# Performance work log

Measured on AMD Instinct MI355X. Metric: run time of the kernel, lower is better.

## Reference

```python
import jax, jax.numpy as jnp
import numpy as np

B, CIN, NH, W, L, K = 16, 64, 64, 32, 4, 5
EPS = 1e-5
FORGET_BIAS = 1.0


def conv(x, w, b=None):
    # x: [B,C,H,W], w: [O,I,k,k] -> SAME padding, stride 1 (NCHW)
    y = jax.lax.conv_general_dilated(x, w, (1, 1), 'SAME',
                                     dimension_numbers=('NCHW', 'OIHW', 'NCHW'))
    if b is not None:
        y = y + b[None, :, None, None]
    return y


def ln(x, g, b):
    # torch LayerNorm([C,W,W]): normalize each sample over (C,H,W)
    m = jnp.mean(x, axis=(1, 2, 3), keepdims=True)
    v = jnp.mean((x - m) ** 2, axis=(1, 2, 3), keepdims=True)
    return (x - m) * jax.lax.rsqrt(v + EPS) * g[None] + b[None]


def attn_channel(q, kv):
    # q: [B,C,W,H], kv: [B,L,C,W,H]
    b, c, w, h = q.shape
    qf = q.reshape(b, c, w * h)                 # [B,C,HW]
    kf = kv.reshape(b, -1, w * h)               # [B,L*C,HW]
    a = jax.nn.softmax(jnp.einsum('bcp,blp->bcl', qf, kf), axis=2)  # [B,C,L*C]
    out = jnp.einsum('bcl,blp->bcp', a, kf)     # [B,C,HW]
    return out.reshape(b, c, w, h)


def attn_spatial(q, kv):
    # q: [B,C,W,H], kv: [B,L,C,W,H]
    b, c, w, h = q.shape
    qf = q.reshape(b, c, w * h).transpose(0, 2, 1)          # [B,HW,C]
    kf = kv.transpose(0, 1, 3, 4, 2).reshape(b, -1, c)      # [B,L*HW,C]
    a = jax.nn.softmax(jnp.einsum('bpc,bqc->bpq', qf, kf), axis=2)  # [B,HW,L*HW]
    out = jnp.einsum('bpq,bqc->bpc', a, kf)                 # [B,HW,C]
    return out.reshape(b, w, h, c).transpose(0, 3, 1, 2)


def setup_inputs() -> dict:
    key = jax.random.key(0)
    ks = iter(jax.random.split(key, 64))
    rn = lambda shape, s=1.0: jax.random.normal(next(ks), shape, jnp.float32) * s
    ones = lambda shape: jnp.ones(shape, jnp.float32)
    zeros = lambda shape: jnp.zeros(shape, jnp.float32)
    s = 0.02
    d = {}
    d['x_t'] = rn((B, CIN, W, W))
    d['h_t'] = rn((B, NH, W, W))
    d['c_t'] = rn((B, NH, W, W))
    d['c_historys'] = rn((B, L, NH, W, W))
    d['m_t'] = rn((B, NH, W, W))
    d['w_x'] = rn((7 * NH, CIN, K, K), s); d['ln_x_g'] = ones((7 * NH, W, W)); d['ln_x_b'] = zeros((7 * NH, W, W))
    d['w_h'] = rn((4 * NH, NH, K, K), s);  d['ln_h_g'] = ones((4 * NH, W, W)); d['ln_h_b'] = zeros((4 * NH, W, W))
    d['w_m'] = rn((3 * NH, NH, K, K), s);  d['ln_m_g'] = ones((3 * NH, W, W)); d['ln_m_b'] = zeros((3 * NH, W, W))
    d['w_o'] = rn((NH, 2 * NH, K, K), s);  d['ln_o_g'] = ones((NH, W, W));     d['ln_o_b'] = zeros((NH, W, W))
    d['w_last'] = rn((NH, 2 * NH, 1, 1), s)
    d['s_norm_g'] = ones((NH, W, W)); d['s_norm_b'] = zeros((NH, W, W))
    d['c_norm_g'] = ones((NH, W, W)); d['c_norm_b'] = zeros((NH, W, W))
    d['ca_w1'] = rn((NH, NH, K, K), s); d['ca_b1'] = zeros((NH,))
    d['ca_ln_g'] = ones((NH, W, W));    d['ca_ln_b'] = zeros((NH, W, W))
    d['ca_w2'] = rn((NH, NH, 1, 1), s); d['ca_b2'] = zeros((NH,))
    d['sa_w1'] = rn((NH, NH, K, K), s)
    d['sa_ln_g'] = ones((NH, W, W));    d['sa_ln_b'] = zeros((NH, W, W))
    d['sa_w2'] = rn((NH, NH, 1, 1), s)
    d['attn_w'] = rn((NH, NH, 1, 1), s)
    return d


def reference(x_t, h_t, c_t, c_historys, m_t,
              w_x, ln_x_g, ln_x_b, w_h, ln_h_g, ln_h_b, w_m, ln_m_g, ln_m_b,
              w_o, ln_o_g, ln_o_b, w_last,
              s_norm_g, s_norm_b, c_norm_g, c_norm_b,
              ca_w1, ca_b1, ca_ln_g, ca_ln_b, ca_w2, ca_b2,
              sa_w1, sa_ln_g, sa_ln_b, sa_w2, attn_w):
    x_concat = ln(conv(x_t, w_x), ln_x_g, ln_x_b)
    h_concat = ln(conv(h_t, w_h), ln_h_g, ln_h_b)
    m_concat = ln(conv(m_t, w_m), ln_m_g, ln_m_b)
    (i_x, f_x, g_x, i_xp, f_xp, g_xp, o_x) = jnp.split(x_concat, 7, axis=1)
    (i_h, f_h, g_h, o_h) = jnp.split(h_concat, 4, axis=1)
    (i_m, f_m, g_m) = jnp.split(m_concat, 3, axis=1)

    i_t = jax.nn.sigmoid(i_x + i_h)
    f_t = jax.nn.sigmoid(f_x + f_h + FORGET_BIAS)
    g_t = jnp.tanh(g_x + g_h)

    # attn_sum_fussion(c_t, query=f_t, keys=c_historys, values=c_historys)
    sp = ln(c_t + attn_spatial(f_t, c_historys), s_norm_g, s_norm_b)
    ch = ln(c_t + attn_channel(f_t, c_historys), c_norm_g, c_norm_b)
    s_a = conv(jax.nn.relu(ln(conv(sp, sa_w1), sa_ln_g, sa_ln_b)), sa_w2)
    c_a = conv(jax.nn.relu(ln(conv(ch, ca_w1, ca_b1), ca_ln_g, ca_ln_b)), ca_w2, ca_b2)
    attn = conv(s_a + c_a, attn_w)
    c_new = attn + i_t * g_t

    i_tp = jax.nn.sigmoid(i_xp + i_m)
    f_tp = jax.nn.sigmoid(f_xp + f_m + FORGET_BIAS)
    g_tp = jnp.tanh(g_xp + g_m)
    m_new = f_tp * m_t + i_tp * g_tp

    mem = jnp.concatenate((c_new, m_new), axis=1)
    o_t = jax.nn.sigmoid(o_x + o_h + ln(conv(mem, w_o), ln_o_g, ln_o_b))
    h_new = o_t * jnp.tanh(conv(mem, w_last))
    return h_new, c_new, m_new
```

## Files before the change

kernel.cpp:

```cpp
#include <hip/hip_runtime.h>
#include <hip/hip_bf16.h>

#define N1 (1u << 20)

typedef __attribute__((ext_vector_type(8))) short s8v;
typedef __attribute__((ext_vector_type(4))) float f4v;

static __device__ __forceinline__ float sigm(float x){ return 1.f/(1.f + __expf(-x)); }
static __device__ __forceinline__ float tanh_(float x){ return 1.f - 2.f/(__expf(2.f*x) + 1.f); }

static __device__ __forceinline__ ushort f2b(float f){
  union { float f; uint u; } x; x.f = f;
  uint r = x.u + 0x7FFFu + ((x.u >> 16) & 1u);
  return (ushort)(r >> 16);
}

static __device__ __forceinline__ void red_atomic2(float s, float q, float* d, int b, int t){
  #pragma unroll
  for (int m = 32; m; m >>= 1){ s += __shfl_xor(s, m); q += __shfl_xor(q, m); }
  if ((t & 63) == 0){ atomicAdd(&d[b*2], s); atomicAdd(&d[b*2+1], q); }
}

__global__ __launch_bounds__(256) void k_wprep3(
    const float* __restrict__ sA, ushort* __restrict__ dA, int CoA, int CiA, int nA,
    const float* __restrict__ sB, ushort* __restrict__ dB, int CoB, int CiB, int nB,
    const float* __restrict__ sC, ushort* __restrict__ dC, int CoC, int CiC, int nC,
    float* __restrict__ zs)
{
  if (zs && blockIdx.x == 0) zs[threadIdx.x] = 0.f;
  int idx = blockIdx.x*256 + threadIdx.x;
  const float* s; ushort* d; int Co, Ci;
  if (idx < nA){ s=sA; d=dA; Co=CoA; Ci=CiA; }
  else if ((idx -= nA) < nB){ s=sB; d=dB; Co=CoB; Ci=CiB; }
  else if ((idx -= nB) < nC){ s=sC; d=dC; Co=CoC; Ci=CiC; }
  else return;
  int ci = idx % Ci; int r = idx / Ci; int co = r % Co; int tap = r / Co;
  d[idx] = f2b(s[((size_t)(co*Ci + ci))*25 + tap]);
}

struct PT { const float* s; ushort* d; const float* st; const float* g; const float* bb; };

__global__ __launch_bounds__(256) void k_prepT3(PT ja, PT jb, PT jc, int n0, int n1, float invN)
{
  const int lp = blockIdx.y;
  PT j; int pl;
  if (lp < n0){ j = ja; pl = lp; }
  else if (lp < n0 + n1){ j = jb; pl = lp - n0; }
  else { j = jc; pl = lp - n0 - n1; }
  const float* sp = j.s + ((size_t)pl << 16);
  float mean = 0.f, rstd = 0.f;
  if (j.st){
    float s0 = j.st[pl*2], s1 = j.st[pl*2+1];
    mean = s0*invN; rstd = rsqrtf(s1*invN - mean*mean + 1e-5f);
  }
  const int p0 = blockIdx.x << 6;
  __shared__ __align__(16) float T[64][68];
  const int t = threadIdx.x, c = t >> 2, g4 = t & 3;
  #pragma unroll
  for (int i = 0; i < 4; ++i){
    const int px = (g4 << 4) + (i << 2);
    float4 f = *(const float4*)(sp + ((size_t)c << 10) + p0 + px);
    if (j.st){
      const size_t li = ((size_t)c << 10) + p0 + px;
      float4 gv = *(const float4*)(j.g + li);
      float4 bv = *(const float4*)(j.bb + li);
      f.x = (f.x - mean)*rstd*gv.x + bv.x;
      f.y = (f.y - mean)*rstd*gv.y + bv.y;
      f.z = (f.z - mean)*rstd*gv.z + bv.z;
      f.w = (f.w - mean)*rstd*gv.w + bv.w;
    }
    *(float4*)&T[c][px] = f;
  }
  __syncthreads();
  const int p = t >> 2, c0 = (t & 3) << 4;
  uint w4[8];
  #pragma unroll
  for (int k = 0; k < 8; ++k){
    ushort lo = f2b(T[c0 + 2*k][p]);
    ushort hi = f2b(T[c0 + 2*k + 1][p]);
    w4[k] = (uint)lo | ((uint)hi << 16);
  }
  ushort* dst = j.d + ((((size_t)pl << 10) + p0 + p) << 6) + c0;
  *(uint4*)(dst)     = *(uint4*)&w4[0];
  *(uint4*)(dst + 8) = *(uint4*)&w4[4];
}

__global__ __launch_bounds__(256) void k_prepTm(const float* __restrict__ src, ushort* __restrict__ dT)
{
  const int lp = blockIdx.y;
  const int p0 = blockIdx.x << 6;
  const float* sp = src + ((size_t)lp << 16);
  __shared__ __align__(16) float T[64][68];
  const int t = threadIdx.x, c = t >> 2, g4 = t & 3;
  #pragma unroll
  for (int i = 0; i < 4; ++i){
    const int px = (g4 << 4) + (i << 2);
    *(float4*)&T[c][px] = *(const float4*)(sp + ((size_t)c << 10) + p0 + px);
  }
  __syncthreads();
  const int p = t >> 2, c0 = (t & 3) << 4;
  uint w4[8];
  #pragma unroll
  for (int k = 0; k < 8; ++k)
    w4[k] = (uint)f2b(T[c0 + 2*k][p]) | ((uint)f2b(T[c0 + 2*k + 1][p]) << 16);
  ushort* dst = dT + ((((size_t)(lp >> 1) << 10) + p0 + p) << 7) + ((lp & 1) << 6) + c0;
  *(uint4*)(dst)     = *(uint4*)&w4[0];
  *(uint4*)(dst + 8) = *(uint4*)&w4[4];
}

struct Seg {
  const ushort* inT; const ushort* w; const float* bias;
  float* out; float* ostat;
  int Cin, Cout;
};
struct Segs3 { Seg s[3]; int b1, b2; };

template<int MT, int RPB>
__global__ __launch_bounds__(256, MT==4 ? 2 : 3) void k_convX(Segs3 Sg)
{
  constexpr int CO   = MT*16;
  constexpr int NW   = 5*CO*4;
  constexpr int ITW  = (NW + 255) / 256;
  constexpr int DXSH = (MT == 4 ? 8 : 7);
  constexpr int PXB  = 32/RPB;
  constexpr int ROWS = RPB + 4;
  constexpr int RPW  = RPB/4;
  constexpr int NTIL = RPB/2;
  constexpr int SUN2 = ROWS*36;

  const int b = blockIdx.y;
  const int cog = blockIdx.x / PXB, pxblk = blockIdx.x % PXB;
  const int si = (cog >= Sg.b1) + (cog >= Sg.b2);
  const Seg sg = Sg.s[si];
  const int base = si == 0 ? 0 : (si == 1 ? Sg.b1 : Sg.b2);
  const int co0 = (cog - base) * CO;
  const int r0 = pxblk * RPB;
  const int t = threadIdx.x, w = t >> 6, l = t & 63;
  const int lane16 = l & 15, quad = l >> 4;

  __shared__ __align__(16) ushort S_[4][ROWS][36][8];
  __shared__ __align__(16) ushort W_[2][5*CO*32];

  f4v acc[MT][NTIL];
  #pragma unroll
  for (int mi = 0; mi < MT; ++mi)
    #pragma unroll
    for (int n = 0; n < NTIL; ++n) acc[mi][n] = (f4v){0.f,0.f,0.f,0.f};

  size_t woff0[ITW];
  #pragma unroll
  for (int it = 0; it < ITW; ++it){
    const int u = t + it*256;
    const int l16u = u & 15, qu = (u >> 4) & 3;
    const int miu = (u >> 6) & (MT - 1), dxu = u >> DXSH;
    woff0[it] = ((size_t)(dxu*sg.Cout + co0 + miu*16 + l16u))*sg.Cin + (qu << 3);
  }
  const size_t wdy = (size_t)5 * sg.Cout * sg.Cin;

  const int ncc = sg.Cin >> 5;
  for (int cc = 0; cc < ncc; ++cc){
    __syncthreads();
    for (int idx = t; idx < SUN2; idx += 256){
      const int row = idx / 36, col = idx - row*36;
      const int ir = r0 - 2 + row, ic = col - 2;
      uint4 pk[4] = {make_uint4(0,0,0,0),make_uint4(0,0,0,0),make_uint4(0,0,0,0),make_uint4(0,0,0,0)};
      if ((unsigned)ir < 32u && (unsigned)ic < 32u){
        const ushort* bp = sg.inT + ((size_t)((b << 10) + (ir << 5) + ic)) * sg.Cin + (cc << 5);
        #pragma unroll
        for (int q = 0; q < 4; ++q) pk[q] = *(const uint4*)(bp + (q << 3));
      }
      #pragma unroll
      for (int q = 0; q < 4; ++q) *(uint4*)&S_[q][row][col][0] = pk[q];
    }
    {
      uint4 wreg[ITW];
      #pragma unroll
      for (int it = 0; it < ITW; ++it)
        if (ITW*256 == NW || t + it*256 < NW)
          wreg[it] = *(const uint4*)(sg.w + woff0[it] + (cc << 5));
      #pragma unroll
      for (int it = 0; it < ITW; ++it)
        if (ITW*256 == NW || t + it*256 < NW)
          *(uint4*)&W_[0][(size_t)(t + it*256) * 8] = wreg[it];
    }
    __syncthreads();
    #pragma unroll
    for (int dy = 0; dy < 5; ++dy){
      uint4 nreg[ITW];
      if (dy < 4){
        #pragma unroll
        for (int it = 0; it < ITW; ++it)
          if (ITW*256 == NW || t + it*256 < NW)
            nreg[it] = *(const uint4*)(sg.w + woff0[it] + (size_t)(dy+1)*wdy + (cc << 5));
      }
      #pragma unroll
      for (int dx = 0; dx < 5; ++dx){
        s8v a[MT];
        #pragma unroll
        for (int mi = 0; mi < MT; ++mi){
          const int au = ((((dx*MT + mi) << 2) + quad) << 4) + lane16;
          a[mi] = *(const s8v*)&W_[dy & 1][au << 3];
        }
        #pragma unroll
        for (int n = 0; n < NTIL; ++n){
          const int srow = w*RPW + (n >> 1) + dy;
          const int col = ((n & 1) << 4) + lane16 + dx;
          s8v bb = *(const s8v*)&S_[quad][srow][col][0];
          #pragma unroll
          for (int mi = 0; mi < MT; ++mi)
            acc[mi][n] = __builtin_amdgcn_mfma_f32_16x16x32_bf16(a[mi], bb, acc[mi][n], 0, 0, 0);
        }
      }
      if (dy < 4){
        #pragma unroll
        for (int it = 0; it < ITW; ++it)
          if (ITW*256 == NW || t + it*256 < NW)
            *(uint4*)&W_[(dy+1) & 1][(size_t)(t + it*256) * 8] = nreg[it];
      }
      __syncthreads();
    }
  }
  float lsum = 0.f, lsq = 0.f;
  #pragma unroll
  for (int mi = 0; mi < MT; ++mi){
    const int co = co0 + mi*16 + (quad << 2);
    #pragma unroll
    for (int n = 0; n < NTIL; ++n){
      const int row = r0 + w*RPW + (n >> 1);
      const int col = ((n & 1) << 4) + lane16;
      #pragma unroll
      for (int i = 0; i < 4; ++i){
        float v = acc[mi][n][i] + (sg.bias ? sg.bias[co+i] : 0.f);
        sg.out[(((size_t)(b*sg.Cout + co + i)) << 10) + (row << 5) + col] = v;
        lsum += v; lsq += v*v;
      }
    }
  }
  if (sg.ostat) red_atomic2(lsum, lsq, sg.ostat, b, t);
}

__global__ __launch_bounds__(256) void k_prep2(
    const float* __restrict__ sA, ushort* __restrict__ cA, ushort* __restrict__ tA, int nA,
    const float* __restrict__ sB, ushort* __restrict__ cB, ushort* __restrict__ tB)
{
  const int plane = blockIdx.y;
  const float* src; ushort* outC; ushort* outT; int pl;
  if (plane < nA){ src = sA; outC = cA; outT = tA; pl = plane; }
  else { src = sB; outC = cB; outT = tB; pl = plane - nA; }
  const int p0 = blockIdx.x << 6;
  const float* sp = src + ((size_t)pl << 16);
  __shared__ __align__(16) float T[64][68];
  const int t = threadIdx.x, c = t >> 2, g = t & 3;
  #pragma unroll
  for (int i = 0; i < 4; ++i){
    float4 f = *(const float4*)(sp + ((size_t)c << 10) + p0 + (g << 4) + (i << 2));
    *(float4*)&T[c][(g << 4) + (i << 2)] = f;
    uint2 pk2;
    pk2.x = (uint)f2b(f.x) | ((uint)f2b(f.y) << 16);
    pk2.y = (uint)f2b(f.z) | ((uint)f2b(f.w) << 16);
    *(uint2*)(outC + ((((size_t)pl << 6) + c) << 10) + p0 + (g << 4) + (i << 2)) = pk2;
  }
  __syncthreads();
  const int p = t >> 2, c0 = (t & 3) << 4;
  uint w4[8];
  #pragma unroll
  for (int k = 0; k < 8; ++k){
    ushort lo = f2b(T[c0 + 2*k][p]);
    ushort hi = f2b(T[c0 + 2*k + 1][p]);
    w4[k] = (uint)lo | ((uint)hi << 16);
  }
  ushort* dst = outT + ((((size_t)pl << 10) + p0 + p) << 6) + c0;
  *(uint4*)(dst)     = *(uint4*)&w4[0];
  *(uint4*)(dst + 8) = *(uint4*)&w4[4];
}

__global__ __launch_bounds__(256) void k_gates(
    const float* __restrict__ bufx, const float* __restrict__ bufh, const float* __restrict__ bufm,
    const float* __restrict__ lnxg, const float* __restrict__ lnxb,
    const float* __restrict__ lnhg, const float* __restrict__ lnhb,
    const float* __restrict__ lnmg, const float* __restrict__ lnmb,
    const float* __restrict__ m_t, const float* __restrict__ stats,
    float* __restrict__ ft, float* __restrict__ ig, float* __restrict__ osum,
    float* __restrict__ memo, float* __restrict__ out_m)
{
  const int idx = blockIdx.x*256 + threadIdx.x;
  const int b = idx >> 16, rem = idx & 65535;
  const int c = rem >> 10, p = rem & 1023;

  float mx = stats[b*2]      * (1.f/458752.f);
  float vx = stats[b*2+1]    * (1.f/458752.f) - mx*mx;  float rx = rsqrtf(vx + 1e-5f);
  float mh = stats[32+b*2]   * (1.f/262144.f);
  float vh = stats[32+b*2+1] * (1.f/262144.f) - mh*mh;  float rh = rsqrtf(vh + 1e-5f);
  float mm = stats[64+b*2]   * (1.f/196608.f);
  float vm = stats[64+b*2+1] * (1.f/196608.f) - mm*mm;  float rm = rsqrtf(vm + 1e-5f);

  auto LX = [&](int k){
    size_t ch = (size_t)k*64 + c; size_t gi = ((size_t)b*448 + ch)*1024 + p; size_t li = ch*1024 + p;
    return (bufx[gi] - mx)*rx*lnxg[li] + lnxb[li]; };
  auto LH = [&](int k){
    size_t ch = (size_t)k*64 + c; size_t gi = ((size_t)b*256 + ch)*1024 + p; size_t li = ch*1024 + p;
    return (bufh[gi] - mh)*rh*lnhg[li] + lnhb[li]; };
  auto LM = [&](int k){
    size_t ch = (size_t)k*64 + c; size_t gi = ((size_t)b*192 + ch)*1024 + p; size_t li = ch*1024 + p;
    return (bufm[gi] - mm)*rm*lnmg[li] + lnmb[li]; };

  float i_t = sigm(LX(0) + LH(0));
  float f_t = sigm(LX(1) + LH(1) + 1.f);
  float g_t = tanh_(LX(2) + LH(2));
  float i_p = sigm(LX(3) + LM(0));
  float f_p = sigm(LX(4) + LM(1) + 1.f);
  float g_p = tanh_(LX(5) + LM(2));
  float ox = LX(6), oh = LH(3);

  ft[idx]   = f_t;
  ig[idx]   = i_t * g_t;
  osum[idx] = ox + oh;
  float mn = f_p * m_t[idx] + i_p * g_p;
  out_m[idx] = mn;
  memo[((size_t)(b*128 + 64 + c) << 10) + p] = mn;
}

__global__ __launch_bounds__(256) void k_spat_mfma(
    const ushort* __restrict__ qT, const ushort* __restrict__ kvC, const ushort* __restrict__ kvT,
    float* __restrict__ num, float* __restrict__ den)
{
  const int p0 = blockIdx.x << 6, b = blockIdx.y, half = blockIdx.z;
  const int t = threadIdx.x, w = t >> 6, l = t & 63;
  const int lane16 = l & 15, quad = l >> 4;
  __shared__ __align__(16) ushort Kt[64][72];
  __shared__ __align__(16) ushort Kc[64][72];
  __shared__ __align__(16) ushort Eb[64][72];
  __shared__ __align__(16) float  XO[64][65];

  s8v qa0, qa1;
  {
    const ushort* qr = qT + ((((size_t)b << 10) + p0 + (w << 4) + lane16) << 6) + (quad << 3);
    qa0 = *(const s8v*)(qr);
    qa1 = *(const s8v*)(qr + 32);
  }
  f4v o0 = {0.f,0.f,0.f,0.f}, o1 = o0, o2 = o0, o3 = o0, dacc = o0;
  const short oneb = (short)0x3F80;
  const s8v ones = { oneb, oneb, oneb, oneb, oneb, oneb, oneb, oneb };

  const int r = t >> 2, g4 = (t & 3) << 4;
  for (int ck = 0; ck < 16; ++ck){
    const int chunk = (half << 4) + ck;
    const int lidx = chunk >> 4, pk = (chunk & 15) << 6;
    __syncthreads();
    {
      const ushort* sc = kvC + ((((size_t)(b*4 + lidx) << 6) + r) << 10) + pk + g4;
      *(uint4*)&Kc[r][g4]     = *(const uint4*)(sc);
      *(uint4*)&Kc[r][g4 + 8] = *(const uint4*)(sc + 8);
      const ushort* st = kvT + ((((size_t)(b*4 + lidx) << 10) + pk + r) << 6) + g4;
      *(uint4*)&Kt[r][g4]     = *(const uint4*)(st);
      *(uint4*)&Kt[r][g4 + 8] = *(const uint4*)(st + 8);
    }
    __syncthreads();
    #pragma unroll
    for (int nt = 0; nt < 4; ++nt){
      const ushort* bt = &Kt[(nt << 4) + lane16][quad << 3];
      s8v b0 = *(const s8v*)(bt);
      s8v b1 = *(const s8v*)(bt + 32);
      f4v s = {0.f,0.f,0.f,0.f};
      s = __builtin_amdgcn_mfma_f32_16x16x32_bf16(qa0, b0, s, 0, 0, 0);
      s = __builtin_amdgcn_mfma_f32_16x16x32_bf16(qa1, b1, s, 0, 0, 0);
      #pragma unroll
      for (int i = 0; i < 4; ++i){
        float e = __expf(s[i] - 12.f);
        Eb[(w << 4) + (quad << 2) + i][(nt << 4) + lane16] = f2b(e);
      }
    }
    __syncthreads();
    #pragma unroll
    for (int ks = 0; ks < 2; ++ks){
      s8v ea = *(const s8v*)&Eb[(w << 4) + lane16][(ks << 5) + (quad << 3)];
      dacc = __builtin_amdgcn_mfma_f32_16x16x32_bf16(ea, ones, dacc, 0, 0, 0);
      s8v bc0 = *(const s8v*)&Kc[ 0 + lane16][(ks << 5) + (quad << 3)];
      s8v bc1 = *(const s8v*)&Kc[16 + lane16][(ks << 5) + (quad << 3)];
      s8v bc2 = *(const s8v*)&Kc[32 + lane16][(ks << 5) + (quad << 3)];
      s8v bc3 = *(const s8v*)&Kc[48 + lane16][(ks << 5) + (quad << 3)];
      o0 = __builtin_amdgcn_mfma_f32_16x16x32_bf16(ea, bc0, o0, 0, 0, 0);
      o1 = __builtin_amdgcn_mfma_f32_16x16x32_bf16(ea, bc1, o1, 0, 0, 0);
      o2 = __builtin_amdgcn_mfma_f32_16x16x32_bf16(ea, bc2, o2, 0, 0, 0);
      o3 = __builtin_amdgcn_mfma_f32_16x16x32_bf16(ea, bc3, o3, 0, 0, 0);
    }
  }
  {
    const int pxl = (w << 4) + (quad << 2);
    if (lane16 == 0){
      float* dp = den + (((size_t)(half*16 + b)) << 10) + p0 + pxl;
      dp[0] = dacc[0]; dp[1] = dacc[1]; dp[2] = dacc[2]; dp[3] = dacc[3];
    }
    XO[ 0 + lane16][pxl+0] = o0[0]; XO[ 0 + lane16][pxl+1] = o0[1];
    XO[ 0 + lane16][pxl+2] = o0[2]; XO[ 0 + lane16][pxl+3] = o0[3];
    XO[16 + lane16][pxl+0] = o1[0]; XO[16 + lane16][pxl+1] = o1[1];
    XO[16 + lane16][pxl+2] = o1[2]; XO[16 + lane16][pxl+3] = o1[3];
    XO[32 + lane16][pxl+0] = o2[0]; XO[32 + lane16][pxl+1] = o2[1];
    XO[32 + lane16][pxl+2] = o2[2]; XO[32 + lane16][pxl+3] = o2[3];
    XO[48 + lane16][pxl+0] = o3[0]; XO[48 + lane16][pxl+1] = o3[1];
    XO[48 + lane16][pxl+2] = o3[2]; XO[48 + lane16][pxl+3] = o3[3];
  }
  __syncthreads();
  {
    const int ch = t >> 2;
    float* nout = num + (size_t)half * N1;
    #pragma unroll
    for (int i = 0; i < 4; ++i){
      size_t gi = ((size_t)b << 16) + ((size_t)ch << 10) + p0 + g4 + (i << 2);
      float4 ov;
      ov.x = XO[ch][g4 + (i << 2) + 0];
      ov.y = XO[ch][g4 + (i << 2) + 1];
      ov.z = XO[ch][g4 + (i << 2) + 2];
      ov.w = XO[ch][g4 + (i << 2) + 3];
      *(float4*)(nout + gi) = ov;
    }
  }
}

__global__ __launch_bounds__(256) void k_spcomb(
    const float* num, const float* __restrict__ den,
    const float* __restrict__ c_t, float* sp_raw, float* __restrict__ stats)
{
  const int p0 = blockIdx.x << 6, b = blockIdx.y, t = threadIdx.x;
  const int ch = t >> 2, g4 = (t & 3) << 4;
  float lsum = 0.f, lsq = 0.f;
  #pragma unroll
  for (int i = 0; i < 4; ++i){
    const int px = p0 + g4 + (i << 2);
    size_t gi = ((size_t)b << 16) + ((size_t)ch << 10) + px;
    float4 ns = {0.f,0.f,0.f,0.f};
    float d0 = 0.f, d1 = 0.f, d2 = 0.f, d3 = 0.f;
    #pragma unroll
    for (int k = 0; k < 4; ++k){
      float4 nk = *(const float4*)(num + (size_t)k*N1 + gi);
      ns.x += nk.x; ns.y += nk.y; ns.z += nk.z; ns.w += nk.w;
      const float* dp = den + (((size_t)(k*16 + b)) << 10) + px;
      d0 += dp[0]; d1 += dp[1]; d2 += dp[2]; d3 += dp[3];
    }
    float4 cv = *(const float4*)(c_t + gi);
    float4 ov;
    ov.x = cv.x + ns.x / d0;
    ov.y = cv.y + ns.y / d1;
    ov.z = cv.z + ns.z / d2;
    ov.w = cv.w + ns.w / d3;
    *(float4*)(sp_raw + gi) = ov;
    lsum += ov.x + ov.y + ov.z + ov.w;
    lsq  += ov.x*ov.x + ov.y*ov.y + ov.z*ov.z + ov.w*ov.w;
  }
  red_atomic2(lsum, lsq, stats, b, t);
}

__global__ __launch_bounds__(256) void k_chlog_m(
    const ushort* __restrict__ ftC, const ushort* __restrict__ kvC, float* __restrict__ lg)
{
  const int bx = blockIdx.x, b = blockIdx.y;
  const int np = bx >> 1, mp = bx & 1;
  const int t = threadIdx.x, w = t >> 6, l = t & 63;
  const int lane16 = l & 15, quad = l >> 4;
  __shared__ __align__(16) ushort As[8][32][8];
  __shared__ __align__(16) ushort Bs[8][64][8];
  f4v acc[2];
  acc[0] = (f4v){0.f,0.f,0.f,0.f}; acc[1] = (f4v){0.f,0.f,0.f,0.f};

  for (int kc = 0; kc < 16; ++kc){
    __syncthreads();
    {
      const int c = t >> 3, q = t & 7;
      *(uint4*)&As[q][c][0] = *(const uint4*)(ftC + (((size_t)(b*64 + mp*32 + c)) << 10) + (kc<<6) + (q<<3));
    }
    #pragma unroll
    for (int it = 0; it < 2; ++it){
      const int idx = t + it*256;
      const int r2 = idx >> 3, q = idx & 7;
      *(uint4*)&Bs[q][r2][0] = *(const uint4*)(kvC + ((((size_t)(b*4 + np) << 6) + r2) << 10) + (kc<<6) + (q<<3));
    }
    __syncthreads();
    #pragma unroll
    for (int ks = 0; ks < 2; ++ks){
      s8v a0 = *(const s8v*)&As[(ks<<2)+quad][lane16][0];
      s8v a1 = *(const s8v*)&As[(ks<<2)+quad][16 + lane16][0];
      s8v bb = *(const s8v*)&Bs[(ks<<2)+quad][(w<<4) + lane16][0];
      acc[0] = __builtin_amdgcn_mfma_f32_16x16x32_bf16(a0, bb, acc[0], 0, 0, 0);
      acc[1] = __builtin_amdgcn_mfma_f32_16x16x32_bf16(a1, bb, acc[1], 0, 0, 0);
    }
  }
  #pragma unroll
  for (int mi = 0; mi < 2; ++mi)
    #pragma unroll
    for (int i = 0; i < 4; ++i){
      const int c = mp*32 + mi*16 + (quad<<2) + i;
      const int n = (np<<6) + (w<<4) + lane16;
      lg[(((size_t)(b*64 + c)) << 8) + n] = acc[mi][i];
    }
}

__global__ __launch_bounds__(256) void k_chsm(const float* __restrict__ a, ushort* __restrict__ ab)
{
  const int row  = blockIdx.x*4 + (threadIdx.x >> 6);
  const int lane = threadIdx.x & 63;
  const float* rp = a + ((size_t)row << 8);
  float v0 = rp[lane], v1 = rp[lane+64], v2 = rp[lane+128], v3 = rp[lane+192];
  float mx = fmaxf(fmaxf(v0, v1), fmaxf(v2, v3));
  #pragma unroll
  for (int m = 32; m; m >>= 1) mx = fmaxf(mx, __shfl_xor(mx, m));
  v0 = __expf(v0 - mx); v1 = __expf(v1 - mx); v2 = __expf(v2 - mx); v3 = __expf(v3 - mx);
  float s = v0 + v1 + v2 + v3;
  #pragma unroll
  for (int m = 32; m; m >>= 1) s += __shfl_xor(s, m);
  float inv = 1.f / s;
  ushort* op = ab + ((size_t)row << 8);
  op[lane] = f2b(v0*inv); op[lane+64] = f2b(v1*inv);
  op[lane+128] = f2b(v2*inv); op[lane+192] = f2b(v3*inv);
}

__global__ __launch_bounds__(256) void k_chout_m(
    const ushort* __restrict__ chlb, const ushort* __restrict__ kvT,
    const float* __restrict__ c_t, float* __restrict__ ch_raw, float* __restrict__ stats)
{
  const int p0 = blockIdx.x << 6, b = blockIdx.y;
  const int t = threadIdx.x, w = t >> 6, l = t & 63;
  const int lane16 = l & 15, quad = l >> 4;
  __shared__ __align__(16) ushort As[32][64][8];
  __shared__ __align__(16) ushort Bs[32][32][8];
  #pragma unroll
  for (int it = 0; it < 8; ++it){
    const int idx = t + it*256;
    const int c = idx >> 5, q = idx & 31;
    *(uint4*)&As[q][c][0] = *(const uint4*)(chlb + (((size_t)(b*64 + c)) << 8) + (q<<3));
  }
  __syncthreads();
  s8v a[8];
  #pragma unroll
  for (int ks = 0; ks < 8; ++ks)
    a[ks] = *(const s8v*)&As[(ks<<2)+quad][(w<<4) + lane16][0];
  float lsum = 0.f, lsq = 0.f;
  for (int pc = 0; pc < 2; ++pc){
    __syncthreads();
    #pragma unroll
    for (int it = 0; it < 4; ++it){
      const int idx = t + it*256;
      const int px = idx >> 5, q = idx & 31;
      const int plane = (b<<2) + (q>>3);
      *(uint4*)&Bs[q][px][0] = *(const uint4*)(kvT + ((((size_t)plane << 10) + p0 + (pc<<5) + px) << 6) + ((q&7)<<3));
    }
    __syncthreads();
    #pragma unroll
    for (int nt = 0; nt < 2; ++nt){
      f4v o = {0.f,0.f,0.f,0.f};
      #pragma unroll
      for (int ks = 0; ks < 8; ++ks){
        s8v bb = *(const s8v*)&Bs[(ks<<2)+quad][(nt<<4) + lane16][0];
        o = __builtin_amdgcn_mfma_f32_16x16x32_bf16(a[ks], bb, o, 0, 0, 0);
      }
      #pragma unroll
      for (int i = 0; i < 4; ++i){
        const int c = (w<<4) + (quad<<2) + i;
        const int px = p0 + (pc<<5) + (nt<<4) + lane16;
        size_t gi = ((size_t)b << 16) + ((size_t)c << 10) + px;
        float v = c_t[gi] + o[i];
        ch_raw[gi] = v;
        lsum += v; lsq += v*v;
      }
    }
  }
  red_atomic2(lsum, lsq, stats, b, t);
}

__global__ __launch_bounds__(256) void k_attnfinal(
    const float* __restrict__ samid, const float* __restrict__ camid,
    const float* __restrict__ stats_sa, const float* __restrict__ stats_ca,
    const float* __restrict__ salng, const float* __restrict__ salnb,
    const float* __restrict__ calng, const float* __restrict__ calnb,
    const float* __restrict__ wsa2, const float* __restrict__ wca2,
    const float* __restrict__ cab2, const float* __restrict__ wat,
    const float* __restrict__ ig, float* __restrict__ out_c, float* __restrict__ memo)
{
  const int p0 = blockIdx.x << 6, b = blockIdx.y, t = threadIdx.x;
  const int tc = t & 15, tp = t >> 4;
  __shared__ __align__(16) float R[64][68];
  __shared__ __align__(16) float Wl[64][68];
  __shared__ __align__(16) float Ms[64][68];
  const float invN = 1.f/65536.f;
  float acc[4][4] = {};
  #pragma unroll
  for (int pass = 0; pass < 2; ++pass){
    const float* mid = pass ? camid : samid;
    const float* st  = pass ? stats_ca : stats_sa;
    const float* g   = pass ? calng : salng;
    const float* bb  = pass ? calnb : salnb;
    const float* w   = pass ? wca2  : wsa2;
    float mean = st[b*2]*invN;
    float var  = st[b*2+1]*invN - mean*mean;
    float rstd = rsqrtf(var + 1e-5f);
    __syncthreads();
    {
      const int j = t & 63, c0 = t >> 6;
      for (int ci = c0; ci < 64; ci += 4){
        size_t gi = ((size_t)b << 16) + ((size_t)ci << 10) + p0 + j;
        size_t li = ((size_t)ci << 10) + p0 + j;
        float v = (mid[gi] - mean)*rstd*g[li] + bb[li];
        R[ci][j] = fmaxf(v, 0.f);
      }
      const int ci2 = t & 63, c20 = t >> 6;
      for (int c2 = c20; c2 < 64; c2 += 4) Wl[ci2][c2] = w[((size_t)c2 << 6) + ci2];
    }
    __syncthreads();
    for (int ci = 0; ci < 64; ++ci){
      float wv[4], rv[4];
      *(float4*)wv = *(const float4*)&Wl[ci][4*tc];
      *(float4*)rv = *(const float4*)&R[ci][4*tp];
      #pragma unroll
      for (int i = 0; i < 4; ++i)
        #pragma unroll
        for (int j = 0; j < 4; ++j)
          acc[i][j] = fmaf(wv[i], rv[j], acc[i][j]);
    }
  }
  {
    float b2[4];
    #pragma unroll
    for (int i = 0; i < 4; ++i) b2[i] = cab2[4*tc + i];
    #pragma unroll
    for (int i = 0; i < 4; ++i)
      #pragma unroll
      for (int j = 0; j < 4; ++j)
        Ms[4*tc+i][4*tp+j] = acc[i][j] + b2[i];
  }
  __syncthreads();
  {
    const int ci2 = t & 63, c20 = t >> 6;
    for (int c2 = c20; c2 < 64; c2 += 4) Wl[ci2][c2] = wat[((size_t)c2 << 6) + ci2];
  }
  __syncthreads();
  float acc2[4][4] = {};
  for (int c2 = 0; c2 < 64; ++c2){
    float wv[4], mv[4];
    *(float4*)wv = *(const float4*)&Wl[c2][4*tc];
    *(float4*)mv = *(const float4*)&Ms[c2][4*tp];
    #pragma unroll
    for (int i = 0; i < 4; ++i)
      #pragma unroll
      for (int j = 0; j < 4; ++j)
        acc2[i][j] = fmaf(wv[i], mv[j], acc2[i][j]);
  }
  #pragma unroll
  for (int i = 0; i < 4; ++i)
    #pragma unroll
    for (int j = 0; j < 4; ++j){
      size_t gi = ((size_t)b << 16) + ((size_t)(4*tc + i) << 10) + p0 + 4*tp + j;
      float v = acc2[i][j] + ig[gi];
      out_c[gi] = v;
      memo[((size_t)(b*128 + 4*tc + i) << 10) + p0 + 4*tp + j] = v;
    }
}

__global__ __launch_bounds__(256) void k_final(
    const float* __restrict__ memo, const float* __restrict__ wlast,
    const float* __restrict__ bufo, const float* __restrict__ osum,
    const float* __restrict__ stats_o, const float* __restrict__ lnog, const float* __restrict__ lnob,
    float* __restrict__ out_h)
{
  const int p0 = blockIdx.x << 6, b = blockIdx.y, t = threadIdx.x;
  const int tc = t & 15, tp = t >> 4;
  __shared__ __align__(16) float Msh[64][68];
  __shared__ __align__(16) float Wt[64][68];
  float acc[4][4] = {};
  #pragma unroll
  for (int half = 0; half < 2; ++half){
    __syncthreads();
    {
      const int j = t & 63, c0 = t >> 6;
      for (int ci = c0; ci < 64; ci += 4)
        Msh[ci][j] = memo[((size_t)(b*128 + half*64 + ci) << 10) + p0 + j];
      const int ci2 = t & 63, co0 = t >> 6;
      for (int co = co0; co < 64; co += 4) Wt[ci2][co] = wlast[((size_t)co << 7) + half*64 + ci2];
    }
    __syncthreads();
    for (int ci = 0; ci < 64; ++ci){
      float wv[4], mv[4];
      *(float4*)wv = *(const float4*)&Wt[ci][4*tc];
      *(float4*)mv = *(const float4*)&Msh[ci][4*tp];
      #pragma unroll
      for (int i = 0; i < 4; ++i)
        #pragma unroll
        for (int j = 0; j < 4; ++j)
          acc[i][j] = fmaf(wv[i], mv[j], acc[i][j]);
    }
  }
  float mean = stats_o[b*2]*(1.f/65536.f);
  float var  = stats_o[b*2+1]*(1.f/65536.f) - mean*mean;
  float rstd = rsqrtf(var + 1e-5f);
  #pragma unroll
  for (int i = 0; i < 4; ++i)
    #pragma unroll
    for (int j = 0; j < 4; ++j){
      const int co = 4*tc + i, p = p0 + 4*tp + j;
      size_t gi = ((size_t)b << 16) + ((size_t)co << 10) + p;
      size_t li = ((size_t)co << 10) + p;
      float lno = (bufo[gi] - mean)*rstd*lnog[li] + lnob[li];
      float o = sigm(osum[gi] + lno);
      out_h[gi] = o * tanh_(acc[i][j]);
    }
}

extern "C" void kernel_launch(void* const* d_in, const int* in_sizes, int n_in,
                              void* d_out, int out_size, void* d_ws, size_t ws_size,
                              hipStream_t stream)
{
  const float* x_t   = (const float*)d_in[0];
  const float* h_t   = (const float*)d_in[1];
  const float* c_t   = (const float*)d_in[2];
  const float* chist = (const float*)d_in[3];
  const float* m_t   = (const float*)d_in[4];
  const float* w_x   = (const float*)d_in[5];
  const float* lnxg  = (const float*)d_in[6];
  const float* lnxb  = (const float*)d_in[7];
  const float* w_h   = (const float*)d_in[8];
  const float* lnhg  = (const float*)d_in[9];
  const float* lnhb  = (const float*)d_in[10];
  const float* w_m   = (const float*)d_in[11];
  const float* lnmg  = (const float*)d_in[12];
  const float* lnmb  = (const float*)d_in[13];
  const float* w_o   = (const float*)d_in[14];
  const float* lnog  = (const float*)d_in[15];
  const float* lnob  = (const float*)d_in[16];
  const float* w_last= (const float*)d_in[17];
  const float* sng   = (const float*)d_in[18];
  const float* snb   = (const float*)d_in[19];
  const float* cng   = (const float*)d_in[20];
  const float* cnb   = (const float*)d_in[21];
  const float* ca_w1 = (const float*)d_in[22];
  const float* ca_b1 = (const float*)d_in[23];
  const float* calng = (const float*)d_in[24];
  const float* calnb = (const float*)d_in[25];
  const float* ca_w2 = (const float*)d_in[26];
  const float* ca_b2 = (const float*)d_in[27];
  const float* sa_w1 = (const float*)d_in[28];
  const float* salng = (const float*)d_in[29];
  const float* salnb = (const float*)d_in[30];
  const float* sa_w2 = (const float*)d_in[31];
  const float* attn_w= (const float*)d_in[32];

  float* out = (float*)d_out;
  float* ws  = (float*)d_ws;

  float* stats = ws;
  float* bufx  = ws + 1024;
  float* bufh  = bufx + 7*(size_t)N1;
  float* bufm  = bufh + 4*(size_t)N1;
  float* ft    = bufm + 3*(size_t)N1;
  float* ig    = ft   + (size_t)N1;
  float* osum  = ig   + (size_t)N1;
  float* memo  = osum + (size_t)N1;
  float* sp    = bufx;
  float* ch    = bufx + (size_t)N1;
  float* samid = bufx + 2*(size_t)N1;
  float* camid = bufx + 3*(size_t)N1;
  float* bufo  = bufx + 4*(size_t)N1;
  float* chl   = bufx + 5*(size_t)N1;
  ushort* kvC  = (ushort*)bufh;
  ushort* kvT  = kvC + 4*(size_t)N1;
  ushort* qT   = (ushort*)bufm;
  ushort* ftC  = qT + (size_t)N1;

  ushort* xT   = (ushort*)memo;
  ushort* hT   = xT + (size_t)N1;
  ushort* mT   = hT + (size_t)N1;
  ushort* spT  = ftC + (size_t)N1;
  ushort* chT  = spT + (size_t)N1;
  float*  numB = bufx;
  float*  denP = chl;
  ushort* memoT = (ushort*)bufx;

  ushort* wbx = (ushort*)ft;
  ushort* wbh = wbx + 716800;
  ushort* wbm = wbh + 409600;
  ushort* wbo  = (ushort*)(chl + 262144);
  ushort* wbsa = wbo + 204800;
  ushort* wbca = wbsa + 102400;
  ushort* chlb = wbca + 102400;

  float* out_h = out;
  float* out_c = out + (size_t)N1;
  float* out_m = out + 2*(size_t)N1;

  k_wprep3<<<dim3(5600), dim3(256), 0, stream>>>(
      w_x, wbx, 448, 64, 716800,
      w_h, wbh, 256, 64, 409600,
      w_m, wbm, 192, 64, 307200, stats);

  {
    PT jx{ x_t, xT, nullptr, nullptr, nullptr };
    PT jh{ h_t, hT, nullptr, nullptr, nullptr };
    PT jm{ m_t, mT, nullptr, nullptr, nullptr };
    k_prepT3<<<dim3(16,48), dim3(256), 0, stream>>>(jx, jh, jm, 16, 16, 0.f);
  }

  {
    Segs3 XHM;
    XHM.s[0] = Seg{ xT, wbx, nullptr, bufx, stats+0,  64, 448 };
    XHM.s[1] = Seg{ hT, wbh, nullptr, bufh, stats+32, 64, 256 };
    XHM.s[2] = Seg{ mT, wbm, nullptr, bufm, stats+64, 64, 192 };
    XHM.b1 = 7; XHM.b2 = 11;
    k_convX<4,8><<<dim3(56,16), dim3(256), 0, stream>>>(XHM);
  }

  k_gates<<<dim3(4096), dim3(256), 0, stream>>>(bufx, bufh, bufm, lnxg, lnxb, lnhg, lnhb,
                                                lnmg, lnmb, m_t, stats,
                                                ft, ig, osum, memo, out_m);

  k_wprep3<<<dim3(1600), dim3(256), 0, stream>>>(
      w_o,   wbo,  64, 128, 204800,
      sa_w1, wbsa, 64,  64, 102400,
      ca_w1, wbca, 64,  64, 102400, nullptr);

  k_prep2<<<dim3(16,80), dim3(256), 0, stream>>>(chist, kvC, kvT, 64, ft, ftC, qT);

  k_spat_mfma<<<dim3(16,16,4), dim3(256), 0, stream>>>(qT, kvC, kvT, numB, denP);
  k_spcomb<<<dim3(16,16), dim3(256), 0, stream>>>(numB, denP, c_t, sp, stats+96);

  k_chlog_m<<<dim3(8,16), dim3(256), 0, stream>>>(ftC, kvC, chl);
  k_chsm  <<<dim3(256),  dim3(256), 0, stream>>>(chl, chlb);
  k_chout_m<<<dim3(16,16), dim3(256), 0, stream>>>(chlb, kvT, c_t, ch, stats+128);

  {
    PT js{ sp, spT, stats+96,  sng, snb };
    PT jc{ ch, chT, stats+128, cng, cnb };
    k_prepT3<<<dim3(16,32), dim3(256), 0, stream>>>(js, jc, js, 16, 16, 1.f/65536.f);
  }

  {
    Segs3 SC;
    SC.s[0] = Seg{ spT, wbsa, nullptr, samid, stats+160, 64, 64 };
    SC.s[1] = Seg{ chT, wbca, ca_b1,   camid, stats+192, 64, 64 };
    SC.s[2] = SC.s[1];
    SC.b1 = 2; SC.b2 = 1000;
    k_convX<2,4><<<dim3(32,16), dim3(256), 0, stream>>>(SC);
  }

  k_attnfinal<<<dim3(16,16), dim3(256), 0, stream>>>(samid, camid, stats+160, stats+192,
                                                     salng, salnb, calng, calnb,
                                                     sa_w2, ca_w2, ca_b2, attn_w,
                                                     ig, out_c, memo);

  k_prepTm<<<dim3(16,32), dim3(256), 0, stream>>>(memo, memoT);

  {
    Segs3 O;
    O.s[0] = Seg{ memoT, wbo, nullptr, bufo, stats+224, 128, 64 };
    O.s[1] = O.s[0]; O.s[2] = O.s[0];
    O.b1 = 1000; O.b2 = 1000;
    k_convX<2,4><<<dim3(16,16), dim3(256), 0, stream>>>(O);
  }

  k_final<<<dim3(16,16), dim3(256), 0, stream>>>(memo, w_last, bufo, osum, stats+224,
                                                 lnog, lnob, out_h);
}
```

Baseline: 501.7 us.

## Merge prep, attention and softmax kernels into fewer launches and fuse memo transpose

Combines the weight-prep and input-transpose kernels into single launches, splits spatial attention across two halves instead of four and co-schedules it with the channel-logit GEMM in one grid, and merges the channel softmax with the spatial combine step. The m_new half of the memo transpose moves into the post-gates prep kernel, and the c_new half is written directly from the attention-final epilogue, which removes the separate transpose launch. The conv tiles for the SA/CA and output convolutions now cover 8 rows per block. The aim is to cut launch overhead and the extra passes over intermediate buffers. In exchange there are fewer blocks in some grids, so parallelism drops, and the heterogeneous blocks in each merged grid may be unevenly loaded.

```diff
diff --git a/kernel.cpp b/kernel.cpp
--- a/kernel.cpp
+++ b/kernel.cpp
@@ -21,21 +21,116 @@
   if ((t & 63) == 0){ atomicAdd(&d[b*2], s); atomicAdd(&d[b*2+1], q); }
 }
 
-__global__ __launch_bounds__(256) void k_wprep3(
-    const float* __restrict__ sA, ushort* __restrict__ dA, int CoA, int CiA, int nA,
-    const float* __restrict__ sB, ushort* __restrict__ dB, int CoB, int CiB, int nB,
-    const float* __restrict__ sC, ushort* __restrict__ dC, int CoC, int CiC, int nC,
+__global__ __launch_bounds__(256) void k_pre(
+    const float* __restrict__ wX, ushort* __restrict__ dX,
+    const float* __restrict__ wH, ushort* __restrict__ dH,
+    const float* __restrict__ wM, ushort* __restrict__ dM,
+    const float* __restrict__ x_t, ushort* __restrict__ xT,
+    const float* __restrict__ h_t, ushort* __restrict__ hT,
+    const float* __restrict__ m_t, ushort* __restrict__ mT,
     float* __restrict__ zs)
 {
-  if (zs && blockIdx.x == 0) zs[threadIdx.x] = 0.f;
-  int idx = blockIdx.x*256 + threadIdx.x;
-  const float* s; ushort* d; int Co, Ci;
-  if (idx < nA){ s=sA; d=dA; Co=CoA; Ci=CiA; }
-  else if ((idx -= nA) < nB){ s=sB; d=dB; Co=CoB; Ci=CiB; }
-  else if ((idx -= nB) < nC){ s=sC; d=dC; Co=CoC; Ci=CiC; }
-  else return;
-  int ci = idx % Ci; int r = idx / Ci; int co = r % Co; int tap = r / Co;
-  d[idx] = f2b(s[((size_t)(co*Ci + ci))*25 + tap]);
+  const int bid = blockIdx.x, t = threadIdx.x;
+  __shared__ __align__(16) float T[64][68];
+  if (bid < 5600){
+    if (bid == 0) zs[t] = 0.f;
+    int idx = bid*256 + t;
+    const float* s; ushort* d; int Co;
+    if (idx < 716800){ s=wX; d=dX; Co=448; }
+    else if ((idx -= 716800) < 409600){ s=wH; d=dH; Co=256; }
+    else if ((idx -= 409600) < 307200){ s=wM; d=dM; Co=192; }
+    else return;
+    int ci = idx & 63; int r = idx >> 6; int co = r % Co; int tap = r / Co;
+    d[idx] = f2b(s[((size_t)(co*64 + ci))*25 + tap]);
+    return;
+  }
+  const int j = bid - 5600;
+  const int p0 = (j & 15) << 6;
+  const int lp = j >> 4;
+  const float* src; ushort* outT; int pl;
+  if (lp < 16){ src = x_t; outT = xT; pl = lp; }
+  else if (lp < 32){ src = h_t; outT = hT; pl = lp - 16; }
+  else { src = m_t; outT = mT; pl = lp - 32; }
+  const float* sp = src + ((size_t)pl << 16);
+  const int c = t >> 2, g = t & 3;
+  #pragma unroll
+  for (int i = 0; i < 4; ++i)
+    *(float4*)&T[c][(g<<4)+(i<<2)] = *(const float4*)(sp + ((size_t)c << 10) + p0 + (g<<4) + (i<<2));
+  __syncthreads();
+  const int p = t >> 2, c0 = (t & 3) << 4;
+  uint w4[8];
+  #pragma unroll
+  for (int k = 0; k < 8; ++k)
+    w4[k] = (uint)f2b(T[c0+2*k][p]) | ((uint)f2b(T[c0+2*k+1][p]) << 16);
+  ushort* dst = outT + ((((size_t)pl << 10) + p0 + p) << 6) + c0;
+  *(uint4*)(dst)     = *(uint4*)&w4[0];
+  *(uint4*)(dst + 8) = *(uint4*)&w4[4];
+}
+
+__global__ __launch_bounds__(256) void k_postgates(
+    const float* __restrict__ wO, ushort* __restrict__ dO,
+    const float* __restrict__ wSA, ushort* __restrict__ dSA,
+    const float* __restrict__ wCA, ushort* __restrict__ dCA,
+    const float* __restrict__ chist, ushort* __restrict__ kvC, ushort* __restrict__ kvT,
+    const float* __restrict__ ft, ushort* __restrict__ ftC, ushort* __restrict__ qT,
+    const float* __restrict__ memo, ushort* __restrict__ memoT)
+{
+  const int bid = blockIdx.x, t = threadIdx.x;
+  __shared__ __align__(16) float T[64][68];
+  if (bid < 1600){
+    int idx = bid*256 + t;
+    const float* s; ushort* d; int Co, Ci;
+    if (idx < 204800){ s=wO; d=dO; Co=64; Ci=128; }
+    else if ((idx -= 204800) < 102400){ s=wSA; d=dSA; Co=64; Ci=64; }
+    else if ((idx -= 102400) < 102400){ s=wCA; d=dCA; Co=64; Ci=64; }
+    else return;
+    int ci = idx % Ci; int r = idx / Ci; int co = r % Co; int tap = r / Co;
+    d[idx] = f2b(s[((size_t)(co*Ci + ci))*25 + tap]);
+    return;
+  }
+  const int j = bid - 1600;
+  const int p0 = (j & 15) << 6;
+  const int lp = j >> 4;
+  const int c = t >> 2, g = t & 3;
+  if (lp < 80){
+    const float* src; ushort* outC; ushort* outT; int pl;
+    if (lp < 64){ src = chist; outC = kvC; outT = kvT; pl = lp; }
+    else { src = ft; outC = ftC; outT = qT; pl = lp - 64; }
+    const float* sp = src + ((size_t)pl << 16);
+    #pragma unroll
+    for (int i = 0; i < 4; ++i){
+      float4 f = *(const float4*)(sp + ((size_t)c << 10) + p0 + (g<<4) + (i<<2));
+      *(float4*)&T[c][(g<<4)+(i<<2)] = f;
+      uint2 pk2;
+      pk2.x = (uint)f2b(f.x) | ((uint)f2b(f.y) << 16);
+      pk2.y = (uint)f2b(f.z) | ((uint)f2b(f.w) << 16);
+      *(uint2*)(outC + ((((size_t)pl << 6) + c) << 10) + p0 + (g<<4) + (i<<2)) = pk2;
+    }
+    __syncthreads();
+    const int p = t >> 2, c0 = (t & 3) << 4;
+    uint w4[8];
+    #pragma unroll
+    for (int k = 0; k < 8; ++k)
+      w4[k] = (uint)f2b(T[c0+2*k][p]) | ((uint)f2b(T[c0+2*k+1][p]) << 16);
+    ushort* dst = outT + ((((size_t)pl << 10) + p0 + p) << 6) + c0;
+    *(uint4*)(dst)     = *(uint4*)&w4[0];
+    *(uint4*)(dst + 8) = *(uint4*)&w4[4];
+  } else {
+    const int b = lp - 80;
+    const float* sp = memo + ((size_t)(b*2 + 1) << 16);
+    #pragma unroll
+    for (int i = 0; i < 4; ++i)
+      *(float4*)&T[c][(g<<4)+(i<<2)] = *(const float4*)(sp + ((size_t)c << 10) + p0 + (g<<4) + (i<<2));
+    __syncthreads();
+    const int p = t >> 2, c0 = (t & 3) << 4;
+    uint w4[8];
+    #pragma unroll
+    for (int k = 0; k < 8; ++k)
+      w4[k] = (uint)f2b(T[c0+2*k][p]) | ((uint)f2b(T[c0+2*k+1][p]) << 16);
+    ushort* dst = memoT + ((((size_t)b << 10) + p0 + p) << 7) + 64 + c0;
+    *(uint4*)(dst)     = *(uint4*)&w4[0];
+    *(uint4*)(dst + 8) = *(uint4*)&w4[4];
+  }
 }
 
 struct PT { const float* s; ushort* d; const float* st; const float* g; const float* bb; };
@@ -81,29 +176,6 @@
     w4[k] = (uint)lo | ((uint)hi << 16);
   }
   ushort* dst = j.d + ((((size_t)pl << 10) + p0 + p) << 6) + c0;
-  *(uint4*)(dst)     = *(uint4*)&w4[0];
-  *(uint4*)(dst + 8) = *(uint4*)&w4[4];
-}
-
-__global__ __launch_bounds__(256) void k_prepTm(const float* __restrict__ src, ushort* __restrict__ dT)
-{
-  const int lp = blockIdx.y;
-  const int p0 = blockIdx.x << 6;
-  const float* sp = src + ((size_t)lp << 16);
-  __shared__ __align__(16) float T[64][68];
-  const int t = threadIdx.x, c = t >> 2, g4 = t & 3;
-  #pragma unroll
-  for (int i = 0; i < 4; ++i){
-    const int px = (g4 << 4) + (i << 2);
-    *(float4*)&T[c][px] = *(const float4*)(sp + ((size_t)c << 10) + p0 + px);
-  }
-  __syncthreads();
-  const int p = t >> 2, c0 = (t & 3) << 4;
-  uint w4[8];
-  #pragma unroll
-  for (int k = 0; k < 8; ++k)
-    w4[k] = (uint)f2b(T[c0 + 2*k][p]) | ((uint)f2b(T[c0 + 2*k + 1][p]) << 16);
-  ushort* dst = dT + ((((size_t)(lp >> 1) << 10) + p0 + p) << 7) + ((lp & 1) << 6) + c0;
   *(uint4*)(dst)     = *(uint4*)&w4[0];
   *(uint4*)(dst + 8) = *(uint4*)&w4[4];
 }
@@ -239,41 +311,6 @@
   if (sg.ostat) red_atomic2(lsum, lsq, sg.ostat, b, t);
 }
 
-__global__ __launch_bounds__(256) void k_prep2(
-    const float* __restrict__ sA, ushort* __restrict__ cA, ushort* __restrict__ tA, int nA,
-    const float* __restrict__ sB, ushort* __restrict__ cB, ushort* __restrict__ tB)
-{
-  const int plane = blockIdx.y;
-  const float* src; ushort* outC; ushort* outT; int pl;
-  if (plane < nA){ src = sA; outC = cA; outT = tA; pl = plane; }
-  else { src = sB; outC = cB; outT = tB; pl = plane - nA; }
-  const int p0 = blockIdx.x << 6;
-  const float* sp = src + ((size_t)pl << 16);
-  __shared__ __align__(16) float T[64][68];
-  const int t = threadIdx.x, c = t >> 2, g = t & 3;
-  #pragma unroll
-  for (int i = 0; i < 4; ++i){
-    float4 f = *(const float4*)(sp + ((size_t)c << 10) + p0 + (g << 4) + (i << 2));
-    *(float4*)&T[c][(g << 4) + (i << 2)] = f;
-    uint2 pk2;
-    pk2.x = (uint)f2b(f.x) | ((uint)f2b(f.y) << 16);
-    pk2.y = (uint)f2b(f.z) | ((uint)f2b(f.w) << 16);
-    *(uint2*)(outC + ((((size_t)pl << 6) + c) << 10) + p0 + (g << 4) + (i << 2)) = pk2;
-  }
-  __syncthreads();
-  const int p = t >> 2, c0 = (t & 3) << 4;
-  uint w4[8];
-  #pragma unroll
-  for (int k = 0; k < 8; ++k){
-    ushort lo = f2b(T[c0 + 2*k][p]);
-    ushort hi = f2b(T[c0 + 2*k + 1][p]);
-    w4[k] = (uint)lo | ((uint)hi << 16);
-  }
-  ushort* dst = outT + ((((size_t)pl << 10) + p0 + p) << 6) + c0;
-  *(uint4*)(dst)     = *(uint4*)&w4[0];
-  *(uint4*)(dst + 8) = *(uint4*)&w4[4];
-}
-
 __global__ __launch_bounds__(256) void k_gates(
     const float* __restrict__ bufx, const float* __restrict__ bufh, const float* __restrict__ bufm,
     const float* __restrict__ lnxg, const float* __restrict__ lnxb,
@@ -320,197 +357,195 @@
   memo[((size_t)(b*128 + 64 + c) << 10) + p] = mn;
 }
 
-__global__ __launch_bounds__(256) void k_spat_mfma(
+__global__ __launch_bounds__(256) void k_spat_chlog(
     const ushort* __restrict__ qT, const ushort* __restrict__ kvC, const ushort* __restrict__ kvT,
-    float* __restrict__ num, float* __restrict__ den)
-{
-  const int p0 = blockIdx.x << 6, b = blockIdx.y, half = blockIdx.z;
-  const int t = threadIdx.x, w = t >> 6, l = t & 63;
+    float* __restrict__ num, float* __restrict__ den,
+    const ushort* __restrict__ ftC, float* __restrict__ lg)
+{
+  __shared__ __align__(16) char smem[44288];
+  const int bid = blockIdx.x, t = threadIdx.x;
+  const int w = t >> 6, l = t & 63;
   const int lane16 = l & 15, quad = l >> 4;
-  __shared__ __align__(16) ushort Kt[64][72];
-  __shared__ __align__(16) ushort Kc[64][72];
-  __shared__ __align__(16) ushort Eb[64][72];
-  __shared__ __align__(16) float  XO[64][65];
-
-  s8v qa0, qa1;
-  {
-    const ushort* qr = qT + ((((size_t)b << 10) + p0 + (w << 4) + lane16) << 6) + (quad << 3);
-    qa0 = *(const s8v*)(qr);
-    qa1 = *(const s8v*)(qr + 32);
-  }
-  f4v o0 = {0.f,0.f,0.f,0.f}, o1 = o0, o2 = o0, o3 = o0, dacc = o0;
-  const short oneb = (short)0x3F80;
-  const s8v ones = { oneb, oneb, oneb, oneb, oneb, oneb, oneb, oneb };
-
-  const int r = t >> 2, g4 = (t & 3) << 4;
-  for (int ck = 0; ck < 16; ++ck){
-    const int chunk = (half << 4) + ck;
-    const int lidx = chunk >> 4, pk = (chunk & 15) << 6;
-    __syncthreads();
+
+  if (bid < 512){
+    const int p0 = (bid & 15) << 6, b = (bid >> 4) & 15, half = bid >> 8;
+    ushort (*Kt)[72] = reinterpret_cast<ushort(*)[72]>(smem);
+    ushort (*Kc)[72] = reinterpret_cast<ushort(*)[72]>(smem + 9216);
+    ushort (*Eb)[72] = reinterpret_cast<ushort(*)[72]>(smem + 18432);
+    float  (*XO)[65] = reinterpret_cast<float(*)[65]>(smem + 27648);
+
+    s8v qa0, qa1;
     {
-      const ushort* sc = kvC + ((((size_t)(b*4 + lidx) << 6) + r) << 10) + pk + g4;
-      *(uint4*)&Kc[r][g4]     = *(const uint4*)(sc);
-      *(uint4*)&Kc[r][g4 + 8] = *(const uint4*)(sc + 8);
-      const ushort* st = kvT + ((((size_t)(b*4 + lidx) << 10) + pk + r) << 6) + g4;
-      *(uint4*)&Kt[r][g4]     = *(const uint4*)(st);
-      *(uint4*)&Kt[r][g4 + 8] = *(const uint4*)(st + 8);
-    }
-    __syncthreads();
-    #pragma unroll
-    for (int nt = 0; nt < 4; ++nt){
-      const ushort* bt = &Kt[(nt << 4) + lane16][quad << 3];
-      s8v b0 = *(const s8v*)(bt);
-      s8v b1 = *(const s8v*)(bt + 32);
-      f4v s = {0.f,0.f,0.f,0.f};
-      s = __builtin_amdgcn_mfma_f32_16x16x32_bf16(qa0, b0, s, 0, 0, 0);
-      s = __builtin_amdgcn_mfma_f32_16x16x32_bf16(qa1, b1, s, 0, 0, 0);
+      const ushort* qr = qT + ((((size_t)b << 10) + p0 + (w << 4) + lane16) << 6) + (quad << 3);
+      qa0 = *(const s8v*)(qr);
+      qa1 = *(const s8v*)(qr + 32);
+    }
+    f4v o0 = {0.f,0.f,0.f,0.f}, o1 = o0, o2 = o0, o3 = o0, dacc = o0;
+    const short oneb = (short)0x3F80;
+    const s8v ones = { oneb, oneb, oneb, oneb, oneb, oneb, oneb, oneb };
+
+    const int r = t >> 2, g4 = (t & 3) << 4;
+    for (int ck = 0; ck < 32; ++ck){
+      const int chunk = (half << 5) + ck;
+      const int lidx = chunk >> 4, pk = (chunk & 15) << 6;
+      __syncthreads();
+      {
+        const ushort* sc = kvC + ((((size_t)(b*4 + lidx) << 6) + r) << 10) + pk + g4;
+        *(uint4*)&Kc[r][g4]     = *(const uint4*)(sc);
+        *(uint4*)&Kc[r][g4 + 8] = *(const uint4*)(sc + 8);
+        const ushort* st = kvT + ((((size_t)(b*4 + lidx) << 10) + pk + r) << 6) + g4;
+        *(uint4*)&Kt[r][g4]     = *(const uint4*)(st);
+        *(uint4*)&Kt[r][g4 + 8] = *(const uint4*)(st + 8);
+      }
+      __syncthreads();
+      #pragma unroll
+      for (int nt = 0; nt < 4; ++nt){
+        const ushort* bt = &Kt[(nt << 4) + lane16][quad << 3];
+        s8v b0 = *(const s8v*)(bt);
+        s8v b1 = *(const s8v*)(bt + 32);
+        f4v s = {0.f,0.f,0.f,0.f};
+        s = __builtin_amdgcn_mfma_f32_16x16x32_bf16(qa0, b0, s, 0, 0, 0);
+        s = __builtin_amdgcn_mfma_f32_16x16x32_bf16(qa1, b1, s, 0, 0, 0);
+        #pragma unroll
+        for (int i = 0; i < 4; ++i){
+          float e = __expf(s[i] - 12.f);
+          Eb[(w << 4) + (quad << 2) + i][(nt << 4) + lane16] = f2b(e);
+        }
+      }
+      __syncthreads();
+      #pragma unroll
+      for (int ks = 0; ks < 2; ++ks){
+        s8v ea = *(const s8v*)&Eb[(w << 4) + lane16][(ks << 5) + (quad << 3)];
+        dacc = __builtin_amdgcn_mfma_f32_16x16x32_bf16(ea, ones, dacc, 0, 0, 0);
+        s8v bc0 = *(const s8v*)&Kc[ 0 + lane16][(ks << 5) + (quad << 3)];
+        s8v bc1 = *(const s8v*)&Kc[16 + lane16][(ks << 5) + (quad << 3)];
+        s8v bc2 = *(const s8v*)&Kc[32 + lane16][(ks << 5) + (quad << 3)];
+        s8v bc3 = *(const s8v*)&Kc[48 + lane16][(ks << 5) + (quad << 3)];
+        o0 = __builtin_amdgcn_mfma_f32_16x16x32_bf16(ea, bc0, o0, 0, 0, 0);
+        o1 = __builtin_amdgcn_mfma_f32_16x16x32_bf16(ea, bc1, o1, 0, 0, 0);
+        o2 = __builtin_amdgcn_mfma_f32_16x16x32_bf16(ea, bc2, o2, 0, 0, 0);
+        o3 = __builtin_amdgcn_mfma_f32_16x16x32_bf16(ea, bc3, o3, 0, 0, 0);
+      }
+    }
+    {
+      const int pxl = (w << 4) + (quad << 2);
+      if (lane16 == 0){
+        float* dp = den + (((size_t)(half*16 + b)) << 10) + p0 + pxl;
+        dp[0] = dacc[0]; dp[1] = dacc[1]; dp[2] = dacc[2]; dp[3] = dacc[3];
+      }
+      XO[ 0 + lane16][pxl+0] = o0[0]; XO[ 0 + lane16][pxl+1] = o0[1];
+      XO[ 0 + lane16][pxl+2] = o0[2]; XO[ 0 + lane16][pxl+3] = o0[3];
+      XO[16 + lane16][pxl+0] = o1[0]; XO[16 + lane16][pxl+1] = o1[1];
+      XO[16 + lane16][pxl+2] = o1[2]; XO[16 + lane16][pxl+3] = o1[3];
+      XO[32 + lane16][pxl+0] = o2[0]; XO[32 + lane16][pxl+1] = o2[1];
+      XO[32 + lane16][pxl+2] = o2[2]; XO[32 + lane16][pxl+3] = o2[3];
+      XO[48 + lane16][pxl+0] = o3[0]; XO[48 + lane16][pxl+1] = o3[1];
+      XO[48 + lane16][pxl+2] = o3[2]; XO[48 + lane16][pxl+3] = o3[3];
+    }
+    __syncthreads();
+    {
+      const int ch = t >> 2;
+      float* nout = num + (size_t)half * N1;
       #pragma unroll
       for (int i = 0; i < 4; ++i){
-        float e = __expf(s[i] - 12.f);
-        Eb[(w << 4) + (quad << 2) + i][(nt << 4) + lane16] = f2b(e);
-      }
-    }
-    __syncthreads();
-    #pragma unroll
-    for (int ks = 0; ks < 2; ++ks){
-      s8v ea = *(const s8v*)&Eb[(w << 4) + lane16][(ks << 5) + (quad << 3)];
-      dacc = __builtin_amdgcn_mfma_f32_16x16x32_bf16(ea, ones, dacc, 0, 0, 0);
-      s8v bc0 = *(const s8v*)&Kc[ 0 + lane16][(ks << 5) + (quad << 3)];
-      s8v bc1 = *(const s8v*)&Kc[16 + lane16][(ks << 5) + (quad << 3)];
-      s8v bc2 = *(const s8v*)&Kc[32 + lane16][(ks << 5) + (quad << 3)];
-      s8v bc3 = *(const s8v*)&Kc[48 + lane16][(ks << 5) + (quad << 3)];
-      o0 = __builtin_amdgcn_mfma_f32_16x16x32_bf16(ea, bc0, o0, 0, 0, 0);
-      o1 = __builtin_amdgcn_mfma_f32_16x16x32_bf16(ea, bc1, o1, 0, 0, 0);
-      o2 = __builtin_amdgcn_mfma_f32_16x16x32_bf16(ea, bc2, o2, 0, 0, 0);
-      o3 = __builtin_amdgcn_mfma_f32_16x16x32_bf16(ea, bc3, o3, 0, 0, 0);
-    }
-  }
-  {
-    const int pxl = (w << 4) + (quad << 2);
-    if (lane16 == 0){
-      float* dp = den + (((size_t)(half*16 + b)) << 10) + p0 + pxl;
-      dp[0] = dacc[0]; dp[1] = dacc[1]; dp[2] = dacc[2]; dp[3] = dacc[3];
-    }
-    XO[ 0 + lane16][pxl+0] = o0[0]; XO[ 0 + lane16][pxl+1] = o0[1];
-    XO[ 0 + lane16][pxl+2] = o0[2]; XO[ 0 + lane16][pxl+3] = o0[3];
-    XO[16 + lane16][pxl+0] = o1[0]; XO[16 + lane16][pxl+1] = o1[1];
-    XO[16 + lane16][pxl+2] = o1[2]; XO[16 + lane16][pxl+3] = o1[3];
-    XO[32 + lane16][pxl+0] = o2[0]; XO[32 + lane16][pxl+1] = o2[1];
-    XO[32 + lane16][pxl+2] = o2[2]; XO[32 + lane16][pxl+3] = o2[3];
-    XO[48 + lane16][pxl+0] = o3[0]; XO[48 + lane16][pxl+1] = o3[1];
-    XO[48 + lane16][pxl+2] = o3[2]; XO[48 + lane16][pxl+3] = o3[3];
-  }
-  __syncthreads();
-  {
-    const int ch = t >> 2;
-    float* nout = num + (size_t)half * N1;
+        size_t gi = ((size_t)b << 16) + ((size_t)ch << 10) + p0 + g4 + (i << 2);
+        float4 ov;
+        ov.x = XO[ch][g4 + (i << 2) + 0];
+        ov.y = XO[ch][g4 + (i << 2) + 1];
+        ov.z = XO[ch][g4 + (i << 2) + 2];
+        ov.w = XO[ch][g4 + (i << 2) + 3];
+        *(float4*)(nout + gi) = ov;
+      }
+    }
+  } else {
+    const int j = bid - 512;
+    const int bx = j & 7, b = j >> 3;
+    const int np = bx >> 1, mp = bx & 1;
+    ushort (*As)[32][8] = reinterpret_cast<ushort(*)[32][8]>(smem);
+    ushort (*Bs)[64][8] = reinterpret_cast<ushort(*)[64][8]>(smem + 4096);
+    f4v acc[2];
+    acc[0] = (f4v){0.f,0.f,0.f,0.f}; acc[1] = (f4v){0.f,0.f,0.f,0.f};
+
+    for (int kc = 0; kc < 16; ++kc){
+      __syncthreads();
+      {
+        const int c = t >> 3, q = t & 7;
+        *(uint4*)&As[q][c][0] = *(const uint4*)(ftC + (((size_t)(b*64 + mp*32 + c)) << 10) + (kc<<6) + (q<<3));
+      }
+      #pragma unroll
+      for (int it = 0; it < 2; ++it){
+        const int idx = t + it*256;
+        const int r2 = idx >> 3, q = idx & 7;
+        *(uint4*)&Bs[q][r2][0] = *(const uint4*)(kvC + ((((size_t)(b*4 + np) << 6) + r2) << 10) + (kc<<6) + (q<<3));
+      }
+      __syncthreads();
+      #pragma unroll
+      for (int ks = 0; ks < 2; ++ks){
+        s8v a0 = *(const s8v*)&As[(ks<<2)+quad][lane16][0];
+        s8v a1 = *(const s8v*)&As[(ks<<2)+quad][16 + lane16][0];
+        s8v bb = *(const s8v*)&Bs[(ks<<2)+quad][(w<<4) + lane16][0];
+        acc[0] = __builtin_amdgcn_mfma_f32_16x16x32_bf16(a0, bb, acc[0], 0, 0, 0);
+        acc[1] = __builtin_amdgcn_mfma_f32_16x16x32_bf16(a1, bb, acc[1], 0, 0, 0);
+      }
+    }
+    #pragma unroll
+    for (int mi = 0; mi < 2; ++mi)
+      #pragma unroll
+      for (int i = 0; i < 4; ++i){
+        const int c = mp*32 + mi*16 + (quad<<2) + i;
+        const int n = (np<<6) + (w<<4) + lane16;
+        lg[(((size_t)(b*64 + c)) << 8) + n] = acc[mi][i];
+      }
+  }
+}
+
+__global__ __launch_bounds__(256) void k_chsm_spcomb(
+    const float* __restrict__ a, ushort* __restrict__ ab,
+    const float* __restrict__ num, const float* __restrict__ den,
+    const float* __restrict__ c_t, float* __restrict__ sp_raw, float* __restrict__ stats)
+{
+  const int bid = blockIdx.x, t = threadIdx.x;
+  if (bid < 256){
+    const int row  = bid*4 + (t >> 6);
+    const int lane = t & 63;
+    const float* rp = a + ((size_t)row << 8);
+    float v0 = rp[lane], v1 = rp[lane+64], v2 = rp[lane+128], v3 = rp[lane+192];
+    float mx = fmaxf(fmaxf(v0, v1), fmaxf(v2, v3));
+    #pragma unroll
+    for (int m = 32; m; m >>= 1) mx = fmaxf(mx, __shfl_xor(mx, m));
+    v0 = __expf(v0 - mx); v1 = __expf(v1 - mx); v2 = __expf(v2 - mx); v3 = __expf(v3 - mx);
+    float s = v0 + v1 + v2 + v3;
+    #pragma unroll
+    for (int m = 32; m; m >>= 1) s += __shfl_xor(s, m);
+    float inv = 1.f / s;
+    ushort* op = ab + ((size_t)row << 8);
+    op[lane] = f2b(v0*inv); op[lane+64] = f2b(v1*inv);
+    op[lane+128] = f2b(v2*inv); op[lane+192] = f2b(v3*inv);
+  } else {
+    const int j = bid - 256;
+    const int p0 = (j & 15) << 6, b = j >> 4;
+    const int ch = t >> 2, g4 = (t & 3) << 4;
+    float lsum = 0.f, lsq = 0.f;
     #pragma unroll
     for (int i = 0; i < 4; ++i){
-      size_t gi = ((size_t)b << 16) + ((size_t)ch << 10) + p0 + g4 + (i << 2);
+      const int px = p0 + g4 + (i << 2);
+      size_t gi = ((size_t)b << 16) + ((size_t)ch << 10) + px;
+      float4 n0 = *(const float4*)(num + gi);
+      float4 n1 = *(const float4*)(num + (size_t)N1 + gi);
+      const float* d0 = den + (((size_t)b) << 10) + px;
+      const float* d1 = den + (((size_t)(16 + b)) << 10) + px;
+      float4 cv = *(const float4*)(c_t + gi);
       float4 ov;
-      ov.x = XO[ch][g4 + (i << 2) + 0];
-      ov.y = XO[ch][g4 + (i << 2) + 1];
-      ov.z = XO[ch][g4 + (i << 2) + 2];
-      ov.w = XO[ch][g4 + (i << 2) + 3];
-      *(float4*)(nout + gi) = ov;
-    }
-  }
-}
-
-__global__ __launch_bounds__(256) void k_spcomb(
-    const float* num, const float* __restrict__ den,
-    const float* __restrict__ c_t, float* sp_raw, float* __restrict__ stats)
-{
-  const int p0 = blockIdx.x << 6, b = blockIdx.y, t = threadIdx.x;
-  const int ch = t >> 2, g4 = (t & 3) << 4;
-  float lsum = 0.f, lsq = 0.f;
-  #pragma unroll
-  for (int i = 0; i < 4; ++i){
-    const int px = p0 + g4 + (i << 2);
-    size_t gi = ((size_t)b << 16) + ((size_t)ch << 10) + px;
-    float4 ns = {0.f,0.f,0.f,0.f};
-    float d0 = 0.f, d1 = 0.f, d2 = 0.f, d3 = 0.f;
-    #pragma unroll
-    for (int k = 0; k < 4; ++k){
-      float4 nk = *(const float4*)(num + (size_t)k*N1 + gi);
-      ns.x += nk.x; ns.y += nk.y; ns.z += nk.z; ns.w += nk.w;
-      const float* dp = den + (((size_t)(k*16 + b)) << 10) + px;
-      d0 += dp[0]; d1 += dp[1]; d2 += dp[2]; d3 += dp[3];
-    }
-    float4 cv = *(const float4*)(c_t + gi);
-    float4 ov;
-    ov.x = cv.x + ns.x / d0;
-    ov.y = cv.y + ns.y / d1;
-    ov.z = cv.z + ns.z / d2;
-    ov.w = cv.w + ns.w / d3;
-    *(float4*)(sp_raw + gi) = ov;
-    lsum += ov.x + ov.y + ov.z + ov.w;
-    lsq  += ov.x*ov.x + ov.y*ov.y + ov.z*ov.z + ov.w*ov.w;
-  }
-  red_atomic2(lsum, lsq, stats, b, t);
-}
-
-__global__ __launch_bounds__(256) void k_chlog_m(
-    const ushort* __restrict__ ftC, const ushort* __restrict__ kvC, float* __restrict__ lg)
-{
-  const int bx = blockIdx.x, b = blockIdx.y;
-  const int np = bx >> 1, mp = bx & 1;
-  const int t = threadIdx.x, w = t >> 6, l = t & 63;
-  const int lane16 = l & 15, quad = l >> 4;
-  __shared__ __align__(16) ushort As[8][32][8];
-  __shared__ __align__(16) ushort Bs[8][64][8];
-  f4v acc[2];
-  acc[0] = (f4v){0.f,0.f,0.f,0.f}; acc[1] = (f4v){0.f,0.f,0.f,0.f};
-
-  for (int kc = 0; kc < 16; ++kc){
-    __syncthreads();
-    {
-      const int c = t >> 3, q = t & 7;
-      *(uint4*)&As[q][c][0] = *(const uint4*)(ftC + (((size_t)(b*64 + mp*32 + c)) << 10) + (kc<<6) + (q<<3));
-    }
-    #pragma unroll
-    for (int it = 0; it < 2; ++it){
-      const int idx = t + it*256;
-      const int r2 = idx >> 3, q = idx & 7;
-      *(uint4*)&Bs[q][r2][0] = *(const uint4*)(kvC + ((((size_t)(b*4 + np) << 6) + r2) << 10) + (kc<<6) + (q<<3));
-    }
-    __syncthreads();
-    #pragma unroll
-    for (int ks = 0; ks < 2; ++ks){
-      s8v a0 = *(const s8v*)&As[(ks<<2)+quad][lane16][0];
-      s8v a1 = *(const s8v*)&As[(ks<<2)+quad][16 + lane16][0];
-      s8v bb = *(const s8v*)&Bs[(ks<<2)+quad][(w<<4) + lane16][0];
-      acc[0] = __builtin_amdgcn_mfma_f32_16x16x32_bf16(a0, bb, acc[0], 0, 0, 0);
-      acc[1] = __builtin_amdgcn_mfma_f32_16x16x32_bf16(a1, bb, acc[1], 0, 0, 0);
-    }
-  }
-  #pragma unroll
-  for (int mi = 0; mi < 2; ++mi)
-    #pragma unroll
-    for (int i = 0; i < 4; ++i){
-      const int c = mp*32 + mi*16 + (quad<<2) + i;
-      const int n = (np<<6) + (w<<4) + lane16;
-      lg[(((size_t)(b*64 + c)) << 8) + n] = acc[mi][i];
-    }
-}
-
-__global__ __launch_bounds__(256) void k_chsm(const float* __restrict__ a, ushort* __restrict__ ab)
-{
-  const int row  = blockIdx.x*4 + (threadIdx.x >> 6);
-  const int lane = threadIdx.x & 63;
-  const float* rp = a + ((size_t)row << 8);
-  float v0 = rp[lane], v1 = rp[lane+64], v2 = rp[lane+128], v3 = rp[lane+192];
-  float mx = fmaxf(fmaxf(v0, v1), fmaxf(v2, v3));
-  #pragma unroll
-  for (int m = 32; m; m >>= 1) mx = fmaxf(mx, __shfl_xor(mx, m));
-  v0 = __expf(v0 - mx); v1 = __expf(v1 - mx); v2 = __expf(v2 - mx); v3 = __expf(v3 - mx);
-  float s = v0 + v1 + v2 + v3;
-  #pragma unroll
-  for (int m = 32; m; m >>= 1) s += __shfl_xor(s, m);
-  float inv = 1.f / s;
-  ushort* op = ab + ((size_t)row << 8);
-  op[lane] = f2b(v0*inv); op[lane+64] = f2b(v1*inv);
-  op[lane+128] = f2b(v2*inv); op[lane+192] = f2b(v3*inv);
+      ov.x = cv.x + (n0.x + n1.x) / (d0[0] + d1[0]);
+      ov.y = cv.y + (n0.y + n1.y) / (d0[1] + d1[1]);
+      ov.z = cv.z + (n0.z + n1.z) / (d0[2] + d1[2]);
+      ov.w = cv.w + (n0.w + n1.w) / (d0[3] + d1[3]);
+      *(float4*)(sp_raw + gi) = ov;
+      lsum += ov.x + ov.y + ov.z + ov.w;
+      lsq  += ov.x*ov.x + ov.y*ov.y + ov.z*ov.z + ov.w*ov.w;
+    }
+    red_atomic2(lsum, lsq, stats, b, t);
+  }
 }
 
 __global__ __launch_bounds__(256) void k_chout_m(
@@ -573,7 +608,8 @@
     const float* __restrict__ calng, const float* __restrict__ calnb,
     const float* __restrict__ wsa2, const float* __restrict__ wca2,
     const float* __restrict__ cab2, const float* __restrict__ wat,
-    const float* __restrict__ ig, float* __restrict__ out_c, float* __restrict__ memo)
+    const float* __restrict__ ig, float* __restrict__ out_c, float* __restrict__ memo,
+    ushort* __restrict__ memoT)
 {
   const int p0 = blockIdx.x << 6, b = blockIdx.y, t = threadIdx.x;
   const int tc = t & 15, tp = t >> 4;
@@ -643,15 +679,24 @@
       for (int j = 0; j < 4; ++j)
         acc2[i][j] = fmaf(wv[i], mv[j], acc2[i][j]);
   }
+  float vv[4][4];
   #pragma unroll
   for (int i = 0; i < 4; ++i)
     #pragma unroll
     for (int j = 0; j < 4; ++j){
       size_t gi = ((size_t)b << 16) + ((size_t)(4*tc + i) << 10) + p0 + 4*tp + j;
       float v = acc2[i][j] + ig[gi];
+      vv[i][j] = v;
       out_c[gi] = v;
       memo[((size_t)(b*128 + 4*tc + i) << 10) + p0 + 4*tp + j] = v;
     }
+  #pragma unroll
+  for (int j = 0; j < 4; ++j){
+    uint2 pk;
+    pk.x = (uint)f2b(vv[0][j]) | ((uint)f2b(vv[1][j]) << 16);
+    pk.y = (uint)f2b(vv[2][j]) | ((uint)f2b(vv[3][j]) << 16);
+    *(uint2*)(memoT + ((((size_t)b << 10) + p0 + 4*tp + j) << 7) + 4*tc) = pk;
+  }
 }
 
 __global__ __launch_bounds__(256) void k_final(
@@ -768,9 +813,8 @@
   ushort* mT   = hT + (size_t)N1;
   ushort* spT  = ftC + (size_t)N1;
   ushort* chT  = spT + (size_t)N1;
+  ushort* memoT = chT + (size_t)N1;
   float*  numB = bufx;
-  float*  denP = chl;
-  ushort* memoT = (ushort*)bufx;
 
   ushort* wbx = (ushort*)ft;
   ushort* wbh = wbx + 716800;
@@ -779,22 +823,14 @@
   ushort* wbsa = wbo + 204800;
   ushort* wbca = wbsa + 102400;
   ushort* chlb = wbca + 102400;
+  float*  denP = chl + 600000;
 
   float* out_h = out;
   float* out_c = out + (size_t)N1;
   float* out_m = out + 2*(size_t)N1;
 
-  k_wprep3<<<dim3(5600), dim3(256), 0, stream>>>(
-      w_x, wbx, 448, 64, 716800,
-      w_h, wbh, 256, 64, 409600,
-      w_m, wbm, 192, 64, 307200, stats);
-
-  {
-    PT jx{ x_t, xT, nullptr, nullptr, nullptr };
-    PT jh{ h_t, hT, nullptr, nullptr, nullptr };
-    PT jm{ m_t, mT, nullptr, nullptr, nullptr };
-    k_prepT3<<<dim3(16,48), dim3(256), 0, stream>>>(jx, jh, jm, 16, 16, 0.f);
-  }
+  k_pre<<<dim3(6368), dim3(256), 0, stream>>>(w_x, wbx, w_h, wbh, w_m, wbm,
+                                              x_t, xT, h_t, hT, m_t, mT, stats);
 
   {
     Segs3 XHM;
@@ -809,18 +845,14 @@
                                                 lnmg, lnmb, m_t, stats,
                                                 ft, ig, osum, memo, out_m);
 
-  k_wprep3<<<dim3(1600), dim3(256), 0, stream>>>(
-      w_o,   wbo,  64, 128, 204800,
-      sa_w1, wbsa, 64,  64, 102400,
-      ca_w1, wbca, 64,  64, 102400, nullptr);
-
-  k_prep2<<<dim3(16,80), dim3(256), 0, stream>>>(chist, kvC, kvT, 64, ft, ftC, qT);
-
-  k_spat_mfma<<<dim3(16,16,4), dim3(256), 0, stream>>>(qT, kvC, kvT, numB, denP);
-  k_spcomb<<<dim3(16,16), dim3(256), 0, stream>>>(numB, denP, c_t, sp, stats+96);
-
-  k_chlog_m<<<dim3(8,16), dim3(256), 0, stream>>>(ftC, kvC, chl);
-  k_chsm  <<<dim3(256),  dim3(256), 0, stream>>>(chl, chlb);
+  k_postgates<<<dim3(3136), dim3(256), 0, stream>>>(w_o, wbo, sa_w1, wbsa, ca_w1, wbca,
+                                                    chist, kvC, kvT, ft, ftC, qT,
+                                                    memo, memoT);
+
+  k_spat_chlog<<<dim3(640), dim3(256), 0, stream>>>(qT, kvC, kvT, numB, denP, ftC, chl);
+
+  k_chsm_spcomb<<<dim3(512), dim3(256), 0, stream>>>(chl, chlb, numB, denP, c_t, sp, stats+96);
+
   k_chout_m<<<dim3(16,16), dim3(256), 0, stream>>>(chlb, kvT, c_t, ch, stats+128);
 
   {
@@ -835,22 +867,20 @@
     SC.s[1] = Seg{ chT, wbca, ca_b1,   camid, stats+192, 64, 64 };
     SC.s[2] = SC.s[1];
     SC.b1 = 2; SC.b2 = 1000;
-    k_convX<2,4><<<dim3(32,16), dim3(256), 0, stream>>>(SC);
+    k_convX<2,8><<<dim3(16,16), dim3(256), 0, stream>>>(SC);
   }
 
   k_attnfinal<<<dim3(16,16), dim3(256), 0, stream>>>(samid, camid, stats+160, stats+192,
                                                      salng, salnb, calng, calnb,
                                                      sa_w2, ca_w2, ca_b2, attn_w,
-                                                     ig, out_c, memo);
-
-  k_prepTm<<<dim3(16,32), dim3(256), 0, stream>>>(memo, memoT);
+                                                     ig, out_c, memo, memoT);
 
   {
     Segs3 O;
     O.s[0] = Seg{ memoT, wbo, nullptr, bufo, stats+224, 128, 64 };
     O.s[1] = O.s[0]; O.s[2] = O.s[0];
     O.b1 = 1000; O.b2 = 1000;
-    k_convX<2,4><<<dim3(16,16), dim3(256), 0, stream>>>(O);
+    k_convX<2,8><<<dim3(8,16), dim3(256), 0, stream>>>(O);
   }
 
   k_final<<<dim3(16,16), dim3(256), 0, stream>>>(memo, w_last, bufo, osum, stats+224,
```

New measurement: 471.2 us, median of 2. 6.1% less time.
